# Kernel optimization log

Measured on AMD Instinct MI355X. Metric: run time of the kernel, lower is better.

Reference implementation:

```python
import jax, jax.numpy as jnp
import numpy as np

EXPERT_NUM = 64
EXPERT_USE = 8
AUX_LOSS_LAMBDA = 0.01


def setup_inputs() -> dict:
    key = jax.random.key(0)
    k1, k2 = jax.random.split(key)
    h = jax.random.normal(k1, (4, 4096, 2048), dtype=jnp.float32)
    # nn.Linear(embed_dim, expert_num) weight: [expert_num, embed_dim], ~U(-1/sqrt(d), 1/sqrt(d))
    bound = 1.0 / np.sqrt(2048.0)
    W = jax.random.uniform(k2, (EXPERT_NUM, 2048), dtype=jnp.float32,
                           minval=-bound, maxval=bound)
    return {"h": h, "W": W}


def reference(h, W):
    b, s, d = h.shape
    hf = h.reshape(-1, d)                              # [b*s, d]
    logits = jnp.einsum('nd,ed->ne', hf, W)            # [b*s, E]
    scores = jax.nn.softmax(logits, axis=-1)           # [b*s, E]
    expert_scores, expert_ids = jax.lax.top_k(scores, EXPERT_USE)  # [b*s, k]
    expert_weight = expert_scores / jnp.sum(expert_scores, axis=-1, keepdims=True)
    # L2 load-balance aux loss (training mode, lambda > 0)
    seq_probs = scores.reshape(b, s, EXPERT_NUM).mean(axis=1)      # [b, E]
    aux_loss = jnp.mean(jnp.sum(seq_probs ** 2, axis=-1)) * EXPERT_NUM * AUX_LOSS_LAMBDA
    return expert_ids, expert_weight, aux_loss
```

## Files before the change

### kernel.cpp

```cpp
#include <hip/hip_runtime.h>
#include <math.h>

#define NTOK 16384
#define DIM 2048
#define NEXP 64
#define TOPK 8
#define BT 32
#define KC 16
#define NCHUNK (DIM / KC)
#define PADK 20
#define NBLK (NTOK / BT)

__global__ __launch_bounds__(256) void moe_gate_np(
    const float* __restrict__ h, const float* __restrict__ W,
    float* __restrict__ out, float* __restrict__ wsum)
{
#pragma clang fp contract(off)
    __shared__ float sA[BT * PADK];
    __shared__ float sB[NEXP * PADK];
    __shared__ float lg[BT][NEXP + 2];

    const int tid = threadIdx.x;
    const int blk = blockIdx.x;
    const long tok0 = (long)blk * BT;
    const float* hA = h + tok0 * DIM;

    const int sr = tid >> 2;
    const int sc = (tid & 3) * 4;

    float4 pa, pb;
    pb = *(const float4*)(W + (long)sr * DIM + sc);
    if (tid < 128) pa = *(const float4*)(hA + (long)sr * DIM + sc);

    const int tx = tid & 15;
    const int ty = tid >> 4;

    float4 c[2][4];
    #pragma unroll
    for (int i = 0; i < 2; ++i)
        #pragma unroll
        for (int j = 0; j < 4; ++j) c[i][j] = make_float4(0.f, 0.f, 0.f, 0.f);

    for (int kc = 0; kc < NCHUNK; ++kc) {
        __syncthreads();
        *(float4*)&sB[sr * PADK + sc] = pb;
        if (tid < 128) *(float4*)&sA[sr * PADK + sc] = pa;
        __syncthreads();

        if (kc + 1 < NCHUNK) {
            const long ko = (long)(kc + 1) * KC;
            pb = *(const float4*)(W + (long)sr * DIM + ko + sc);
            if (tid < 128) pa = *(const float4*)(hA + (long)sr * DIM + ko + sc);
        }

        float4 A[2][4], B[4][4];
        #pragma unroll
        for (int i = 0; i < 2; ++i) {
            const float* base = &sA[(ty + 16 * i) * PADK];
            #pragma unroll
            for (int v = 0; v < 4; ++v) A[i][v] = *(const float4*)(base + 4 * v);
        }
        #pragma unroll
        for (int j = 0; j < 4; ++j) {
            const float* base = &sB[(tx + 16 * j) * PADK];
            #pragma unroll
            for (int v = 0; v < 4; ++v) B[j][v] = *(const float4*)(base + 4 * v);
        }

        #pragma unroll
        for (int i = 0; i < 2; ++i)
            #pragma unroll
            for (int j = 0; j < 4; ++j) {
                float4& cc = c[i][j];
                float t;
                t = A[i][3].x * B[j][3].x + cc.x;
                t = A[i][2].x * B[j][2].x + t;
                t = A[i][1].x * B[j][1].x + t;
                cc.x = A[i][0].x * B[j][0].x + t;
                t = A[i][3].y * B[j][3].y + cc.y;
                t = A[i][2].y * B[j][2].y + t;
                t = A[i][1].y * B[j][1].y + t;
                cc.y = A[i][0].y * B[j][0].y + t;
                t = A[i][3].z * B[j][3].z + cc.z;
                t = A[i][2].z * B[j][2].z + t;
                t = A[i][1].z * B[j][1].z + t;
                cc.z = A[i][0].z * B[j][0].z + t;
                t = A[i][3].w * B[j][3].w + cc.w;
                t = A[i][2].w * B[j][2].w + t;
                t = A[i][1].w * B[j][1].w + t;
                cc.w = A[i][0].w * B[j][0].w + t;
            }
    }

    #pragma unroll
    for (int i = 0; i < 2; ++i)
        #pragma unroll
        for (int j = 0; j < 4; ++j) {
            const float4 v = c[i][j];
            lg[ty + 16 * i][tx + 16 * j] = (v.x + v.z) + (v.y + v.w);
        }
    __syncthreads();

    const int lane = tid & 63;
    const int wv   = tid >> 6;
    float auxacc = 0.f;

    for (int tt = 0; tt < 8; ++tt) {
        const int t = wv * 8 + tt;
        const float s = lg[t][lane];

        float m = s;
        #pragma unroll
        for (int off = 32; off >= 1; off >>= 1)
            m = fmaxf(m, __shfl_xor(m, off));

        const float p = expf(s - m);
        lg[t][lane] = p;
        __asm__ volatile("" ::: "memory");

        float r0 = lg[t][0], r1 = lg[t][1], r2 = lg[t][2], r3 = lg[t][3];
        float r4 = lg[t][4], r5 = lg[t][5], r6 = lg[t][6], r7 = lg[t][7];
        #pragma unroll
        for (int i = 1; i < 8; ++i) {
            r0 += lg[t][8 * i + 0]; r1 += lg[t][8 * i + 1];
            r2 += lg[t][8 * i + 2]; r3 += lg[t][8 * i + 3];
            r4 += lg[t][8 * i + 4]; r5 += lg[t][8 * i + 5];
            r6 += lg[t][8 * i + 6]; r7 += lg[t][8 * i + 7];
        }
        const float S = ((r0 + r1) + (r2 + r3)) + ((r4 + r5) + (r6 + r7));

        const float score = p / S;
        auxacc += score;

        float cv = score;
        float myv = 0.f;
        int   myi = 0;
        #pragma unroll
        for (int i = 0; i < TOPK; ++i) {
            float v = cv;
            int idx = lane;
            #pragma unroll
            for (int off = 32; off >= 1; off >>= 1) {
                float v2 = __shfl_xor(v, off);
                int   i2 = __shfl_xor(idx, off);
                if (v2 > v || (v2 == v && i2 < idx)) { v = v2; idx = i2; }
            }
            if (lane == i)   { myv = v; myi = idx; }
            if (lane == idx) cv = -1.f;
        }

        float S8 = 0.f;
        #pragma unroll
        for (int r = 0; r < TOPK; ++r) S8 += __shfl(myv, r);

        if (lane < TOPK) {
            const long o = (tok0 + t) * TOPK + lane;
            out[o]                     = (float)myi;
            out[(long)NTOK * TOPK + o] = myv / S8;
        }
    }

    const int b = blk >> 7;
    atomicAdd(&wsum[b * NEXP + lane], auxacc);
}

__global__ void aux_finish(const float* __restrict__ wsum, float* __restrict__ out)
{
    const int lane = threadIdx.x;
    float a = 0.f;
    #pragma unroll
    for (int b = 0; b < 4; ++b) {
        const float v = wsum[b * NEXP + lane] * (1.0f / 4096.0f);
        a = fmaf(v, v, a);
    }
    #pragma unroll
    for (int off = 32; off >= 1; off >>= 1)
        a += __shfl_xor(a, off);
    if (lane == 0)
        out[2L * NTOK * TOPK] = a * 0.25f * (float)NEXP * 0.01f;
}

extern "C" void kernel_launch(void* const* d_in, const int* in_sizes, int n_in,
                              void* d_out, int out_size, void* d_ws, size_t ws_size,
                              hipStream_t stream) {
    const float* h = (const float*)d_in[0];
    const float* W = (const float*)d_in[1];
    float* out  = (float*)d_out;
    float* wsum = (float*)d_ws;

    hipMemsetAsync(d_ws, 0, 1024, stream);
    moe_gate_np<<<NBLK, 256, 0, stream>>>(h, W, out, wsum);
    aux_finish<<<1, 64, 0, stream>>>(wsum, out);
}
```

Before: 163.3 us.

## Enlarge K chunk to 64 and use packed FP32 mul/add instructions

Raises the per-iteration K chunk from 16 to 64 so there are a quarter as many barrier/shared-memory staging rounds, and has every thread load more data per chunk. The inner product now uses inline v_pk_mul_f32/v_pk_add_f32 on float2 pairs, keeping separate multiply and add (no FMA contraction) so the rounding order matches the previous code. Launch bounds now request two blocks per CU. The larger shared tiles and prefetch registers raise LDS and register pressure, and the inline asm may limit compiler scheduling.

Measured after the change: 165.5 us. Within noise of the previous version (+1.3%).

```diff
diff --git a/kernel.cpp b/kernel.cpp
--- a/kernel.cpp
+++ b/kernel.cpp
@@ -6,12 +6,22 @@
 #define NEXP 64
 #define TOPK 8
 #define BT 32
-#define KC 16
+#define KC 64
 #define NCHUNK (DIM / KC)
-#define PADK 20
+#define PADK 68
 #define NBLK (NTOK / BT)
 
-__global__ __launch_bounds__(256) void moe_gate_np(
+typedef float f2 __attribute__((ext_vector_type(2)));
+typedef float f4 __attribute__((ext_vector_type(4)));
+
+__device__ __forceinline__ f2 pk_mul(f2 a, f2 b) {
+    f2 d; asm("v_pk_mul_f32 %0, %1, %2" : "=v"(d) : "v"(a), "v"(b)); return d;
+}
+__device__ __forceinline__ f2 pk_add(f2 a, f2 b) {
+    f2 d; asm("v_pk_add_f32 %0, %1, %2" : "=v"(d) : "v"(a), "v"(b)); return d;
+}
+
+__global__ __launch_bounds__(256, 2) void moe_gate_np(
     const float* __restrict__ h, const float* __restrict__ W,
     float* __restrict__ out, float* __restrict__ wsum)
 {
@@ -25,79 +35,88 @@
     const long tok0 = (long)blk * BT;
     const float* hA = h + tok0 * DIM;
 
-    const int sr = tid >> 2;
-    const int sc = (tid & 3) * 4;
-
-    float4 pa, pb;
-    pb = *(const float4*)(W + (long)sr * DIM + sc);
-    if (tid < 128) pa = *(const float4*)(hA + (long)sr * DIM + sc);
+    const int rA = tid >> 3;
+    const int cA = (tid & 7) * 8;
+    const int rB = tid >> 2;
+    const int cB = (tid & 3) * 16;
+
+    f4 pa[2], pb[4];
+    #pragma unroll
+    for (int q = 0; q < 2; ++q) pa[q] = *(const f4*)(hA + (long)rA * DIM + cA + 4 * q);
+    #pragma unroll
+    for (int q = 0; q < 4; ++q) pb[q] = *(const f4*)(W + (long)rB * DIM + cB + 4 * q);
 
     const int tx = tid & 15;
     const int ty = tid >> 4;
 
-    float4 c[2][4];
+    f2 axy[2][4], azw[2][4];
     #pragma unroll
     for (int i = 0; i < 2; ++i)
         #pragma unroll
-        for (int j = 0; j < 4; ++j) c[i][j] = make_float4(0.f, 0.f, 0.f, 0.f);
+        for (int j = 0; j < 4; ++j) { axy[i][j] = (f2)(0.f); azw[i][j] = (f2)(0.f); }
 
     for (int kc = 0; kc < NCHUNK; ++kc) {
         __syncthreads();
-        *(float4*)&sB[sr * PADK + sc] = pb;
-        if (tid < 128) *(float4*)&sA[sr * PADK + sc] = pa;
+        #pragma unroll
+        for (int q = 0; q < 2; ++q) *(f4*)&sA[rA * PADK + cA + 4 * q] = pa[q];
+        #pragma unroll
+        for (int q = 0; q < 4; ++q) *(f4*)&sB[rB * PADK + cB + 4 * q] = pb[q];
         __syncthreads();
 
         if (kc + 1 < NCHUNK) {
             const long ko = (long)(kc + 1) * KC;
-            pb = *(const float4*)(W + (long)sr * DIM + ko + sc);
-            if (tid < 128) pa = *(const float4*)(hA + (long)sr * DIM + ko + sc);
-        }
-
-        float4 A[2][4], B[4][4];
-        #pragma unroll
-        for (int i = 0; i < 2; ++i) {
-            const float* base = &sA[(ty + 16 * i) * PADK];
-            #pragma unroll
-            for (int v = 0; v < 4; ++v) A[i][v] = *(const float4*)(base + 4 * v);
-        }
+            #pragma unroll
+            for (int q = 0; q < 2; ++q) pa[q] = *(const f4*)(hA + (long)rA * DIM + ko + cA + 4 * q);
+            #pragma unroll
+            for (int q = 0; q < 4; ++q) pb[q] = *(const f4*)(W + (long)rB * DIM + ko + cB + 4 * q);
+        }
+
+        #pragma unroll
+        for (int s = 0; s < 4; ++s) {
+            f2 alo[2][4], ahi[2][4], blo[4][4], bhi[4][4];
+            #pragma unroll
+            for (int i = 0; i < 2; ++i) {
+                const float* base = &sA[(ty + 16 * i) * PADK + s * 16];
+                #pragma unroll
+                for (int v = 0; v < 4; ++v) {
+                    f4 a = *(const f4*)(base + 4 * v);
+                    alo[i][v] = __builtin_shufflevector(a, a, 0, 1);
+                    ahi[i][v] = __builtin_shufflevector(a, a, 2, 3);
+                }
+            }
+            #pragma unroll
+            for (int j = 0; j < 4; ++j) {
+                const float* base = &sB[(tx + 16 * j) * PADK + s * 16];
+                #pragma unroll
+                for (int v = 0; v < 4; ++v) {
+                    f4 b = *(const f4*)(base + 4 * v);
+                    blo[j][v] = __builtin_shufflevector(b, b, 0, 1);
+                    bhi[j][v] = __builtin_shufflevector(b, b, 2, 3);
+                }
+            }
+            #pragma unroll
+            for (int i = 0; i < 2; ++i)
+                #pragma unroll
+                for (int j = 0; j < 4; ++j) {
+                    f2 t;
+                    t = pk_add(pk_mul(alo[i][3], blo[j][3]), axy[i][j]);
+                    t = pk_add(pk_mul(alo[i][2], blo[j][2]), t);
+                    t = pk_add(pk_mul(alo[i][1], blo[j][1]), t);
+                    axy[i][j] = pk_add(pk_mul(alo[i][0], blo[j][0]), t);
+                    t = pk_add(pk_mul(ahi[i][3], bhi[j][3]), azw[i][j]);
+                    t = pk_add(pk_mul(ahi[i][2], bhi[j][2]), t);
+                    t = pk_add(pk_mul(ahi[i][1], bhi[j][1]), t);
+                    azw[i][j] = pk_add(pk_mul(ahi[i][0], bhi[j][0]), t);
+                }
+        }
+    }
+
+    #pragma unroll
+    for (int i = 0; i < 2; ++i)
         #pragma unroll
         for (int j = 0; j < 4; ++j) {
-            const float* base = &sB[(tx + 16 * j) * PADK];
-            #pragma unroll
-            for (int v = 0; v < 4; ++v) B[j][v] = *(const float4*)(base + 4 * v);
-        }
-
-        #pragma unroll
-        for (int i = 0; i < 2; ++i)
-            #pragma unroll
-            for (int j = 0; j < 4; ++j) {
-                float4& cc = c[i][j];
-                float t;
-                t = A[i][3].x * B[j][3].x + cc.x;
-                t = A[i][2].x * B[j][2].x + t;
-                t = A[i][1].x * B[j][1].x + t;
-                cc.x = A[i][0].x * B[j][0].x + t;
-                t = A[i][3].y * B[j][3].y + cc.y;
-                t = A[i][2].y * B[j][2].y + t;
-                t = A[i][1].y * B[j][1].y + t;
-                cc.y = A[i][0].y * B[j][0].y + t;
-                t = A[i][3].z * B[j][3].z + cc.z;
-                t = A[i][2].z * B[j][2].z + t;
-                t = A[i][1].z * B[j][1].z + t;
-                cc.z = A[i][0].z * B[j][0].z + t;
-                t = A[i][3].w * B[j][3].w + cc.w;
-                t = A[i][2].w * B[j][2].w + t;
-                t = A[i][1].w * B[j][1].w + t;
-                cc.w = A[i][0].w * B[j][0].w + t;
-            }
-    }
-
-    #pragma unroll
-    for (int i = 0; i < 2; ++i)
-        #pragma unroll
-        for (int j = 0; j < 4; ++j) {
-            const float4 v = c[i][j];
-            lg[ty + 16 * i][tx + 16 * j] = (v.x + v.z) + (v.y + v.w);
+            f2 s2 = pk_add(axy[i][j], azw[i][j]);
+            lg[ty + 16 * i][tx + 16 * j] = s2.x + s2.y;
         }
     __syncthreads();
 
```

## Restructure gate GEMM: wave-uniform W loads from global, 64-token tiles

Applied to the files above, without the earlier changes.

The GEMM is reorganised so each of 8 waves owns 8 experts and reads W rows directly from global memory with wave-uniform addresses, which should become scalar or broadcast loads. Only the activation tile goes through shared memory now, with a larger K chunk of 64 and a 64-token block, and each lane computes one token. The block grows to 512 threads with launch bounds forcing one block per CU, and the aux-loss batch index is adjusted for the new block count. The aim is to remove the LDS traffic and syncs for W and to amortise h loads over a larger K chunk. The risk is lower occupancy and reliance on W reads being served from cache.

New measurement: 263.1 us. 1.61x slower.

```diff
diff --git a/kernel.cpp b/kernel.cpp
--- a/kernel.cpp
+++ b/kernel.cpp
@@ -5,104 +5,102 @@
 #define DIM 2048
 #define NEXP 64
 #define TOPK 8
-#define BT 32
-#define KC 16
+#define BT 64
+#define KC 64
 #define NCHUNK (DIM / KC)
-#define PADK 20
+#define PADK 68
 #define NBLK (NTOK / BT)
+#define EPW 8
 
-__global__ __launch_bounds__(256) void moe_gate_np(
+typedef float f4 __attribute__((ext_vector_type(4)));
+
+__global__ __launch_bounds__(512, 1) void moe_gate_np(
     const float* __restrict__ h, const float* __restrict__ W,
     float* __restrict__ out, float* __restrict__ wsum)
 {
 #pragma clang fp contract(off)
     __shared__ float sA[BT * PADK];
-    __shared__ float sB[NEXP * PADK];
     __shared__ float lg[BT][NEXP + 2];
 
-    const int tid = threadIdx.x;
-    const int blk = blockIdx.x;
+    const int tid  = threadIdx.x;
+    const int blk  = blockIdx.x;
+    const int lane = tid & 63;
+    const int wv   = tid >> 6;
     const long tok0 = (long)blk * BT;
     const float* hA = h + tok0 * DIM;
 
-    const int sr = tid >> 2;
-    const int sc = (tid & 3) * 4;
+    const int ewv = __builtin_amdgcn_readfirstlane(wv);
+    const float* wbase = W + (long)ewv * EPW * DIM;
 
-    float4 pa, pb;
-    pb = *(const float4*)(W + (long)sr * DIM + sc);
-    if (tid < 128) pa = *(const float4*)(hA + (long)sr * DIM + sc);
+    const int i0 = tid,        r0 = i0 >> 4, c0 = (i0 & 15) * 4;
+    const int i1 = tid + 512,  r1 = i1 >> 4, c1 = (i1 & 15) * 4;
 
-    const int tx = tid & 15;
-    const int ty = tid >> 4;
+    f4 pa0 = *(const f4*)(hA + (long)r0 * DIM + c0);
+    f4 pa1 = *(const f4*)(hA + (long)r1 * DIM + c1);
 
-    float4 c[2][4];
+    float acc[EPW][4];
     #pragma unroll
-    for (int i = 0; i < 2; ++i)
+    for (int j = 0; j < EPW; ++j)
         #pragma unroll
-        for (int j = 0; j < 4; ++j) c[i][j] = make_float4(0.f, 0.f, 0.f, 0.f);
+        for (int m = 0; m < 4; ++m) acc[j][m] = 0.f;
 
     for (int kc = 0; kc < NCHUNK; ++kc) {
         __syncthreads();
-        *(float4*)&sB[sr * PADK + sc] = pb;
-        if (tid < 128) *(float4*)&sA[sr * PADK + sc] = pa;
+        *(f4*)&sA[r0 * PADK + c0] = pa0;
+        *(f4*)&sA[r1 * PADK + c1] = pa1;
         __syncthreads();
 
         if (kc + 1 < NCHUNK) {
             const long ko = (long)(kc + 1) * KC;
-            pb = *(const float4*)(W + (long)sr * DIM + ko + sc);
-            if (tid < 128) pa = *(const float4*)(hA + (long)sr * DIM + ko + sc);
-        }
-
-        float4 A[2][4], B[4][4];
-        #pragma unroll
-        for (int i = 0; i < 2; ++i) {
-            const float* base = &sA[(ty + 16 * i) * PADK];
-            #pragma unroll
-            for (int v = 0; v < 4; ++v) A[i][v] = *(const float4*)(base + 4 * v);
-        }
-        #pragma unroll
-        for (int j = 0; j < 4; ++j) {
-            const float* base = &sB[(tx + 16 * j) * PADK];
-            #pragma unroll
-            for (int v = 0; v < 4; ++v) B[j][v] = *(const float4*)(base + 4 * v);
+            pa0 = *(const f4*)(hA + (long)r0 * DIM + ko + c0);
+            pa1 = *(const f4*)(hA + (long)r1 * DIM + ko + c1);
         }
 
         #pragma unroll
-        for (int i = 0; i < 2; ++i)
+        for (int s = 0; s < 4; ++s) {
+            f4 af[4];
+            const float* ab = &sA[lane * PADK + s * 16];
             #pragma unroll
-            for (int j = 0; j < 4; ++j) {
-                float4& cc = c[i][j];
+            for (int v = 0; v < 4; ++v) af[v] = *(const f4*)(ab + 4 * v);
+
+            const int kg = kc * KC + s * 16;
+            #pragma unroll
+            for (int j = 0; j < EPW; ++j) {
+                const float* wr = wbase + (long)j * DIM + kg;
+                const f4 b0 = *(const f4*)(wr);
+                const f4 b1 = *(const f4*)(wr + 4);
+                const f4 b2 = *(const f4*)(wr + 8);
+                const f4 b3 = *(const f4*)(wr + 12);
                 float t;
-                t = A[i][3].x * B[j][3].x + cc.x;
-                t = A[i][2].x * B[j][2].x + t;
-                t = A[i][1].x * B[j][1].x + t;
-                cc.x = A[i][0].x * B[j][0].x + t;
-                t = A[i][3].y * B[j][3].y + cc.y;
-                t = A[i][2].y * B[j][2].y + t;
-                t = A[i][1].y * B[j][1].y + t;
-                cc.y = A[i][0].y * B[j][0].y + t;
-                t = A[i][3].z * B[j][3].z + cc.z;
-                t = A[i][2].z * B[j][2].z + t;
-                t = A[i][1].z * B[j][1].z + t;
-                cc.z = A[i][0].z * B[j][0].z + t;
-                t = A[i][3].w * B[j][3].w + cc.w;
-                t = A[i][2].w * B[j][2].w + t;
-                t = A[i][1].w * B[j][1].w + t;
-                cc.w = A[i][0].w * B[j][0].w + t;
+                t = af[3].x * b3.x + acc[j][0];
+                t = af[2].x * b2.x + t;
+                t = af[1].x * b1.x + t;
+                acc[j][0] = af[0].x * b0.x + t;
+
+                t = af[3].y * b3.y + acc[j][1];
+                t = af[2].y * b2.y + t;
+                t = af[1].y * b1.y + t;
+                acc[j][1] = af[0].y * b0.y + t;
+
+                t = af[3].z * b3.z + acc[j][2];
+                t = af[2].z * b2.z + t;
+                t = af[1].z * b1.z + t;
+                acc[j][2] = af[0].z * b0.z + t;
+
+                t = af[3].w * b3.w + acc[j][3];
+                t = af[2].w * b2.w + t;
+                t = af[1].w * b1.w + t;
+                acc[j][3] = af[0].w * b0.w + t;
             }
+        }
     }
 
+    __syncthreads();
     #pragma unroll
-    for (int i = 0; i < 2; ++i)
-        #pragma unroll
-        for (int j = 0; j < 4; ++j) {
-            const float4 v = c[i][j];
-            lg[ty + 16 * i][tx + 16 * j] = (v.x + v.z) + (v.y + v.w);
-        }
+    for (int j = 0; j < EPW; ++j)
+        lg[lane][wv * EPW + j] = (acc[j][0] + acc[j][2]) + (acc[j][1] + acc[j][3]);
     __syncthreads();
 
-    const int lane = tid & 63;
-    const int wv   = tid >> 6;
     float auxacc = 0.f;
 
     for (int tt = 0; tt < 8; ++tt) {
@@ -118,16 +116,16 @@
         lg[t][lane] = p;
         __asm__ volatile("" ::: "memory");
 
-        float r0 = lg[t][0], r1 = lg[t][1], r2 = lg[t][2], r3 = lg[t][3];
-        float r4 = lg[t][4], r5 = lg[t][5], r6 = lg[t][6], r7 = lg[t][7];
+        float r0s = lg[t][0], r1s = lg[t][1], r2s = lg[t][2], r3s = lg[t][3];
+        float r4s = lg[t][4], r5s = lg[t][5], r6s = lg[t][6], r7s = lg[t][7];
         #pragma unroll
         for (int i = 1; i < 8; ++i) {
-            r0 += lg[t][8 * i + 0]; r1 += lg[t][8 * i + 1];
-            r2 += lg[t][8 * i + 2]; r3 += lg[t][8 * i + 3];
-            r4 += lg[t][8 * i + 4]; r5 += lg[t][8 * i + 5];
-            r6 += lg[t][8 * i + 6]; r7 += lg[t][8 * i + 7];
+            r0s += lg[t][8 * i + 0]; r1s += lg[t][8 * i + 1];
+            r2s += lg[t][8 * i + 2]; r3s += lg[t][8 * i + 3];
+            r4s += lg[t][8 * i + 4]; r5s += lg[t][8 * i + 5];
+            r6s += lg[t][8 * i + 6]; r7s += lg[t][8 * i + 7];
         }
-        const float S = ((r0 + r1) + (r2 + r3)) + ((r4 + r5) + (r6 + r7));
+        const float S = ((r0s + r1s) + (r2s + r3s)) + ((r4s + r5s) + (r6s + r7s));
 
         const float score = p / S;
         auxacc += score;
@@ -160,7 +158,7 @@
         }
     }
 
-    const int b = blk >> 7;
+    const int b = blk >> 6;
     atomicAdd(&wsum[b * NEXP + lane], auxacc);
 }
 
@@ -189,6 +187,6 @@
     float* wsum = (float*)d_ws;
 
     hipMemsetAsync(d_ws, 0, 1024, stream);
-    moe_gate_np<<<NBLK, 256, 0, stream>>>(h, W, out, wsum);
+    moe_gate_np<<<NBLK, 512, 0, stream>>>(h, W, out, wsum);
     aux_finish<<<1, 64, 0, stream>>>(wsum, out);
 }
```
